# Kernel tuning notes

Hardware: AMD Instinct MI355X
Metric: run time of the kernel (lower is better)

Reference implementation:

```python
import jax, jax.numpy as jnp
import numpy as np

NEG = -1e9  # stand-in for -inf in masked softmax (safe under autodiff)

def setup_inputs() -> dict:
    key = jax.random.key(0)
    ks = jax.random.split(key, 10)
    B, Btot, O, M, F, Dsrc, Ddst = 32, 64, 1000, 100, 32, 6, 3
    raw_opes = jax.random.normal(ks[0], (B, O, Dsrc), jnp.float32)
    raw_mas = jax.random.normal(ks[1], (B, M, Ddst), jnp.float32)
    proc_time = jax.random.uniform(ks[2], (B, O, M), jnp.float32)
    ope_ma_adj = jax.random.randint(ks[3], (Btot, O, M), 0, 2).astype(jnp.int64)
    batch_idxes = jnp.sort(jax.random.randint(ks[4], (B,), 0, Btot)).astype(jnp.int64)
    # xavier-ish scaled params
    W_src = jax.random.normal(ks[5], (Dsrc, F), jnp.float32) * (2.0 / np.sqrt(Dsrc + F))
    W_dst = jax.random.normal(ks[6], (Ddst, F), jnp.float32) * (2.0 / np.sqrt(Ddst + F))
    W_edge = jax.random.normal(ks[7], (F,), jnp.float32) * (2.0 / np.sqrt(1 + F))
    attn_l = jax.random.normal(ks[8], (F,), jnp.float32) * (2.0 / np.sqrt(1 + F))
    attn_r = jax.random.normal(ks[9], (F,), jnp.float32) * (2.0 / np.sqrt(1 + F))
    return {"raw_opes": raw_opes, "raw_mas": raw_mas, "proc_time": proc_time,
            "ope_ma_adj": ope_ma_adj, "batch_idxes": batch_idxes,
            "W_src": W_src, "W_dst": W_dst, "W_edge": W_edge,
            "attn_l": attn_l, "attn_r": attn_r}

def _leaky(x, s=0.2):
    return jnp.where(x >= 0, x, s * x)

def reference(raw_opes, raw_mas, proc_time, ope_ma_adj, batch_idxes, W_src, W_dst, W_edge, attn_l, attn_r):
    adj = ope_ma_adj[batch_idxes]                      # [B,O,M] int
    adjf = adj.astype(raw_opes.dtype)
    feat_src = raw_opes @ W_src                        # [B,O,F]
    feat_dst = raw_mas @ W_dst                         # [B,M,F]
    feat_edge = proc_time[..., None] * W_edge          # [B,O,M,F]
    el = feat_src @ attn_l                             # [B,O]
    er = feat_dst @ attn_r                             # [B,M]
    ee = feat_edge @ attn_l                            # [B,O,M]  (original uses attn_l for edges)
    a = adjf * el[:, :, None] + ee + adjf * er[:, None, :]   # [B,O,M]
    eijk = _leaky(a)                                   # [B,O,M]
    ekk = _leaky(er + er)                              # [B,M]
    e = jnp.concatenate([eijk, ekk[:, None, :]], axis=1)     # [B,O+1,M]
    mask = jnp.concatenate([adj == 1, jnp.ones_like(adj[:, :1, :], dtype=bool)], axis=1)
    e = jnp.where(mask, e, NEG)
    alpha = jax.nn.softmax(e, axis=1)                  # softmax over ope dim (+self)
    alpha_ijk = alpha[:, :-1, :]                       # [B,O,M]
    alpha_kk = alpha[:, -1, :]                         # [B,M]
    Wmu_ijk = feat_edge + feat_src[:, :, None, :]      # [B,O,M,F]
    b = jnp.einsum('bomf,bom->bmf', Wmu_ijk, alpha_ijk)
    c = feat_dst * alpha_kk[..., None]
    return jax.nn.sigmoid(b + c)                       # [B,M,F]
```

## Files before the change

kernel.cpp:

```cpp
#include <hip/hip_runtime.h>

#define B_DIM 32
#define O_DIM 1000
#define M_DIM 100
#define F_DIM 32
#define DS 6
#define DD 3
#define SEG 25
#define CHUNK 40
#define OSUB 10
#define TRIPS 4
#define MT 25

__global__ __launch_bounds__(256) void gat_partial(
    const float* __restrict__ raw_opes,
    const float* __restrict__ raw_mas,
    const float* __restrict__ proc_time,
    const int*   __restrict__ adj,
    const int*   __restrict__ bidx,
    const float* __restrict__ Wsrc,
    const float* __restrict__ Wdst,
    const float* __restrict__ Wedge,
    const float* __restrict__ attn_l,
    const float* __restrict__ attn_r,
    float* __restrict__ partial)
{
    const int b   = blockIdx.x / SEG;
    const int seg = blockIdx.x % SEG;
    const int t   = threadIdx.x;
    const int o0  = seg * CHUNK;

    __shared__ float ro_s[CHUNK * DS];
    __shared__ float part_s[OSUB][M_DIM][9];
    __shared__ float wfold[10];

    const int mg = t % 25;
    const int g  = t / 25;

    float4 pt[TRIPS];
    int4   av[TRIPS];
    if (t < 25 * OSUB) {
        const float* ptp = proc_time + ((size_t)b * O_DIM + o0) * M_DIM + mg * 4;
        #pragma unroll
        for (int k = 0; k < TRIPS; ++k)
            pt[k] = *(const float4*)(ptp + (g + k * OSUB) * M_DIM);
        const int* adp = adj + ((size_t)bidx[b] * O_DIM + o0) * M_DIM + mg * 4;
        #pragma unroll
        for (int k = 0; k < TRIPS; ++k)
            av[k] = *(const int4*)(adp + (g + k * OSUB) * M_DIM);
    }

    const float* rop = raw_opes + ((size_t)b * O_DIM + o0) * DS;
    if (t < CHUNK * DS) ro_s[t] = rop[t];

    if (t >= 192) {
        const int l = t - 192;
        const int f = l & 31;
        float al = attn_l[f], ar = attn_r[f];
        float p[10];
        #pragma unroll
        for (int d = 0; d < DS; ++d) p[d] = Wsrc[d * F_DIM + f] * al;
        p[6] = Wedge[f] * al;
        #pragma unroll
        for (int d = 0; d < DD; ++d) p[7 + d] = Wdst[d * F_DIM + f] * ar;
        #pragma unroll
        for (int s = 1; s < 32; s <<= 1) {
            #pragma unroll
            for (int k = 0; k < 10; ++k) p[k] += __shfl_xor(p[k], s);
        }
        if (l == 0) {
            #pragma unroll
            for (int k = 0; k < 10; ++k) wfold[k] = p[k];
        }
    }
    __syncthreads();

    if (t < 25 * OSUB) {
        float wl[DS], wr[DD], we;
        #pragma unroll
        for (int d = 0; d < DS; ++d) wl[d] = wfold[d];
        we = wfold[6];
        #pragma unroll
        for (int d = 0; d < DD; ++d) wr[d] = wfold[7 + d];

        const float* rm = raw_mas + ((size_t)b * M_DIM + mg * 4) * DD;
        float4 er;
        er.x = fmaf(rm[0], wr[0], fmaf(rm[1],  wr[1], rm[2]  * wr[2]));
        er.y = fmaf(rm[3], wr[0], fmaf(rm[4],  wr[1], rm[5]  * wr[2]));
        er.z = fmaf(rm[6], wr[0], fmaf(rm[7],  wr[1], rm[8]  * wr[2]));
        er.w = fmaf(rm[9], wr[0], fmaf(rm[10], wr[1], rm[11] * wr[2]));

        float4 den = make_float4(0, 0, 0, 0), spa = make_float4(0, 0, 0, 0);
        float4 sd[DS];
        #pragma unroll
        for (int d = 0; d < DS; ++d) sd[d] = make_float4(0, 0, 0, 0);

        #pragma unroll
        for (int k = 0; k < TRIPS; ++k) {
            const int row = g + k * OSUB;
            float ro[DS];
            #pragma unroll
            for (int d = 0; d < DS; ++d) ro[d] = ro_s[row * DS + d];
            float elr = 0.f;
            #pragma unroll
            for (int d = 0; d < DS; ++d) elr = fmaf(ro[d], wl[d], elr);

            float s0 = elr + er.x + we * pt[k].x;
            float s1 = elr + er.y + we * pt[k].y;
            float s2 = elr + er.z + we * pt[k].z;
            float s3 = elr + er.w + we * pt[k].w;
            s0 = fmaxf(s0, 0.2f * s0); s1 = fmaxf(s1, 0.2f * s1);
            s2 = fmaxf(s2, 0.2f * s2); s3 = fmaxf(s3, 0.2f * s3);
            float p0 = (av[k].x == 1) ? __expf(s0) : 0.f;
            float p1 = (av[k].y == 1) ? __expf(s1) : 0.f;
            float p2 = (av[k].z == 1) ? __expf(s2) : 0.f;
            float p3 = (av[k].w == 1) ? __expf(s3) : 0.f;
            den.x += p0; den.y += p1; den.z += p2; den.w += p3;
            spa.x = fmaf(p0, pt[k].x, spa.x); spa.y = fmaf(p1, pt[k].y, spa.y);
            spa.z = fmaf(p2, pt[k].z, spa.z); spa.w = fmaf(p3, pt[k].w, spa.w);
            #pragma unroll
            for (int d = 0; d < DS; ++d) {
                sd[d].x = fmaf(p0, ro[d], sd[d].x);
                sd[d].y = fmaf(p1, ro[d], sd[d].y);
                sd[d].z = fmaf(p2, ro[d], sd[d].z);
                sd[d].w = fmaf(p3, ro[d], sd[d].w);
            }
        }

        #pragma unroll
        for (int j = 0; j < 4; ++j) {
            const int m = mg * 4 + j;
            float* ps = part_s[g][m];
            ps[0] = j == 0 ? den.x : j == 1 ? den.y : j == 2 ? den.z : den.w;
            ps[1] = j == 0 ? spa.x : j == 1 ? spa.y : j == 2 ? spa.z : spa.w;
            #pragma unroll
            for (int d = 0; d < DS; ++d)
                ps[2 + d] = j == 0 ? sd[d].x : j == 1 ? sd[d].y : j == 2 ? sd[d].z : sd[d].w;
        }
    }
    __syncthreads();

    if (t < 2 * M_DIM) {
        const int m = t % M_DIM, half = t / M_DIM;
        float a[4] = {0, 0, 0, 0};
        #pragma unroll
        for (int gg = 0; gg < OSUB; ++gg) {
            #pragma unroll
            for (int k = 0; k < 4; ++k) a[k] += part_s[gg][m][half * 4 + k];
        }
        *(float4*)(partial + (((size_t)b * SEG + seg) * M_DIM + m) * 8 + half * 4) =
            make_float4(a[0], a[1], a[2], a[3]);
    }
}

__global__ __launch_bounds__(256) void gat_final(
    const float* __restrict__ raw_mas,
    const float* __restrict__ Wsrc,
    const float* __restrict__ Wdst,
    const float* __restrict__ Wedge,
    const float* __restrict__ attn_r,
    const float* __restrict__ partial,
    float* __restrict__ out)
{
    const int b  = blockIdx.x >> 2;
    const int m0 = (blockIdx.x & 3) * MT;
    const int t  = threadIdx.x;

    __shared__ float smd[MT][9];
    __shared__ float wr_s[DD];

    if (t >= 192) {
        const int l = t - 192;
        const int f = l & 31;
        float ar = attn_r[f];
        float p[DD];
        #pragma unroll
        for (int d = 0; d < DD; ++d) p[d] = Wdst[d * F_DIM + f] * ar;
        #pragma unroll
        for (int s = 1; s < 32; s <<= 1) {
            #pragma unroll
            for (int d = 0; d < DD; ++d) p[d] += __shfl_xor(p[d], s);
        }
        if (l == 0) {
            #pragma unroll
            for (int d = 0; d < DD; ++d) wr_s[d] = p[d];
        }
    }

    if (t < MT * 8) {
        const int ml = t % MT;
        const int k  = t / MT;
        const float* p = partial + (((size_t)b * SEG) * M_DIM + m0 + ml) * 8 + k;
        float acc = 0.f;
        #pragma unroll
        for (int s = 0; s < SEG; ++s) acc += p[(size_t)s * M_DIM * 8];
        smd[ml][k] = acc;
    }
    __syncthreads();

    if (t < MT) {
        const float* rm = raw_mas + ((size_t)b * M_DIM + m0 + t) * DD;
        float er = fmaf(rm[0], wr_s[0], fmaf(rm[1], wr_s[1], rm[2] * wr_s[2]));
        float skk = 2.f * er;
        skk = fmaxf(skk, 0.2f * skk);
        float pkk = __expf(skk);
        float den = smd[t][0], spa = smd[t][1];
        float s0 = smd[t][2], s1 = smd[t][3], s2 = smd[t][4],
              s3 = smd[t][5], s4 = smd[t][6], s5 = smd[t][7];
        float inv = 1.f / (den + pkk);
        smd[t][0] = s0 * inv; smd[t][1] = s1 * inv; smd[t][2] = s2 * inv;
        smd[t][3] = s3 * inv; smd[t][4] = s4 * inv; smd[t][5] = s5 * inv;
        smd[t][6] = spa * inv;
        smd[t][7] = pkk * inv;
    }
    __syncthreads();

    for (int idx = t; idx < MT * F_DIM; idx += 256) {
        const int ml = idx >> 5;
        const int f  = idx & 31;
        float v = smd[ml][6] * Wedge[f];
        #pragma unroll
        for (int d = 0; d < DS; ++d) v = fmaf(smd[ml][d], Wsrc[d * F_DIM + f], v);
        const float* rm = raw_mas + ((size_t)b * M_DIM + m0 + ml) * DD;
        float fd = 0.f;
        #pragma unroll
        for (int d = 0; d < DD; ++d) fd = fmaf(rm[d], Wdst[d * F_DIM + f], fd);
        v = fmaf(fd, smd[ml][7], v);
        out[((size_t)b * M_DIM + m0 + ml) * F_DIM + f] = 1.f / (1.f + __expf(-v));
    }
}

extern "C" void kernel_launch(void* const* d_in, const int* in_sizes, int n_in,
                              void* d_out, int out_size, void* d_ws, size_t ws_size,
                              hipStream_t stream) {
    const float* raw_opes  = (const float*)d_in[0];
    const float* raw_mas   = (const float*)d_in[1];
    const float* proc_time = (const float*)d_in[2];
    const int*   adj       = (const int*)d_in[3];
    const int*   bidx      = (const int*)d_in[4];
    const float* Wsrc      = (const float*)d_in[5];
    const float* Wdst      = (const float*)d_in[6];
    const float* Wedge     = (const float*)d_in[7];
    const float* attn_l    = (const float*)d_in[8];
    const float* attn_r    = (const float*)d_in[9];
    float* out     = (float*)d_out;
    float* partial = (float*)d_ws;

    gat_partial<<<B_DIM * SEG, 256, 0, stream>>>(raw_opes, raw_mas, proc_time, adj, bidx,
                                                 Wsrc, Wdst, Wedge, attn_l, attn_r, partial);
    gat_final<<<B_DIM * 4, 256, 0, stream>>>(raw_mas, Wsrc, Wdst, Wedge, attn_r, partial, out);
}
```

Measured before the change: 17.11 us.

## Reduce segment partials with atomics and flatten final kernel per output element

Each segment block now atomically adds its per-machine partial sums into a zeroed accumulator, replacing the per-segment partial buffer. The memset that zeroes it adds an extra operation to the stream. Segment 0 also writes er to a buffer, so the final kernel becomes a flat one-thread-per-output elementwise pass without shared memory, the cross-segment loop, or the attn_r reduction. The intent is to remove the final kernel's serial 25-way reduction and its synchronisations. In exchange it adds atomic contention on 8 values per (b,m) and makes the floating-point summation order nondeterministic.

Result: slower. 36.25 us (+111.9%).

```diff
diff --git a/kernel.cpp b/kernel.cpp
--- a/kernel.cpp
+++ b/kernel.cpp
@@ -10,7 +10,8 @@
 #define CHUNK 40
 #define OSUB 10
 #define TRIPS 4
-#define MT 25
+#define ACC_BYTES ((size_t)B_DIM * M_DIM * 8 * sizeof(float))
+#define ER_BYTES  ((size_t)B_DIM * M_DIM * sizeof(float))
 
 __global__ __launch_bounds__(256) void gat_partial(
     const float* __restrict__ raw_opes,
@@ -23,7 +24,8 @@
     const float* __restrict__ Wedge,
     const float* __restrict__ attn_l,
     const float* __restrict__ attn_r,
-    float* __restrict__ partial)
+    float* __restrict__ accum,
+    float* __restrict__ er_buf)
 {
     const int b   = blockIdx.x / SEG;
     const int seg = blockIdx.x % SEG;
@@ -89,6 +91,11 @@
         er.y = fmaf(rm[3], wr[0], fmaf(rm[4],  wr[1], rm[5]  * wr[2]));
         er.z = fmaf(rm[6], wr[0], fmaf(rm[7],  wr[1], rm[8]  * wr[2]));
         er.w = fmaf(rm[9], wr[0], fmaf(rm[10], wr[1], rm[11] * wr[2]));
+
+        if (seg == 0 && g == 0) {
+            float* eb = er_buf + (size_t)b * M_DIM + mg * 4;
+            eb[0] = er.x; eb[1] = er.y; eb[2] = er.z; eb[3] = er.w;
+        }
 
         float4 den = make_float4(0, 0, 0, 0), spa = make_float4(0, 0, 0, 0);
         float4 sd[DS];
@@ -148,8 +155,9 @@
             #pragma unroll
             for (int k = 0; k < 4; ++k) a[k] += part_s[gg][m][half * 4 + k];
         }
-        *(float4*)(partial + (((size_t)b * SEG + seg) * M_DIM + m) * 8 + half * 4) =
-            make_float4(a[0], a[1], a[2], a[3]);
+        float* dst = accum + ((size_t)b * M_DIM + m) * 8 + half * 4;
+        #pragma unroll
+        for (int k = 0; k < 4; ++k) atomicAdd(dst + k, a[k]);
     }
 }
 
@@ -158,76 +166,38 @@
     const float* __restrict__ Wsrc,
     const float* __restrict__ Wdst,
     const float* __restrict__ Wedge,
-    const float* __restrict__ attn_r,
-    const float* __restrict__ partial,
+    const float* __restrict__ accum,
+    const float* __restrict__ er_buf,
     float* __restrict__ out)
 {
-    const int b  = blockIdx.x >> 2;
-    const int m0 = (blockIdx.x & 3) * MT;
-    const int t  = threadIdx.x;
-
-    __shared__ float smd[MT][9];
-    __shared__ float wr_s[DD];
-
-    if (t >= 192) {
-        const int l = t - 192;
-        const int f = l & 31;
-        float ar = attn_r[f];
-        float p[DD];
-        #pragma unroll
-        for (int d = 0; d < DD; ++d) p[d] = Wdst[d * F_DIM + f] * ar;
-        #pragma unroll
-        for (int s = 1; s < 32; s <<= 1) {
-            #pragma unroll
-            for (int d = 0; d < DD; ++d) p[d] += __shfl_xor(p[d], s);
-        }
-        if (l == 0) {
-            #pragma unroll
-            for (int d = 0; d < DD; ++d) wr_s[d] = p[d];
-        }
-    }
-
-    if (t < MT * 8) {
-        const int ml = t % MT;
-        const int k  = t / MT;
-        const float* p = partial + (((size_t)b * SEG) * M_DIM + m0 + ml) * 8 + k;
-        float acc = 0.f;
-        #pragma unroll
-        for (int s = 0; s < SEG; ++s) acc += p[(size_t)s * M_DIM * 8];
-        smd[ml][k] = acc;
-    }
-    __syncthreads();
-
-    if (t < MT) {
-        const float* rm = raw_mas + ((size_t)b * M_DIM + m0 + t) * DD;
-        float er = fmaf(rm[0], wr_s[0], fmaf(rm[1], wr_s[1], rm[2] * wr_s[2]));
-        float skk = 2.f * er;
-        skk = fmaxf(skk, 0.2f * skk);
-        float pkk = __expf(skk);
-        float den = smd[t][0], spa = smd[t][1];
-        float s0 = smd[t][2], s1 = smd[t][3], s2 = smd[t][4],
-              s3 = smd[t][5], s4 = smd[t][6], s5 = smd[t][7];
-        float inv = 1.f / (den + pkk);
-        smd[t][0] = s0 * inv; smd[t][1] = s1 * inv; smd[t][2] = s2 * inv;
-        smd[t][3] = s3 * inv; smd[t][4] = s4 * inv; smd[t][5] = s5 * inv;
-        smd[t][6] = spa * inv;
-        smd[t][7] = pkk * inv;
-    }
-    __syncthreads();
-
-    for (int idx = t; idx < MT * F_DIM; idx += 256) {
-        const int ml = idx >> 5;
-        const int f  = idx & 31;
-        float v = smd[ml][6] * Wedge[f];
-        #pragma unroll
-        for (int d = 0; d < DS; ++d) v = fmaf(smd[ml][d], Wsrc[d * F_DIM + f], v);
-        const float* rm = raw_mas + ((size_t)b * M_DIM + m0 + ml) * DD;
-        float fd = 0.f;
-        #pragma unroll
-        for (int d = 0; d < DD; ++d) fd = fmaf(rm[d], Wdst[d * F_DIM + f], fd);
-        v = fmaf(fd, smd[ml][7], v);
-        out[((size_t)b * M_DIM + m0 + ml) * F_DIM + f] = 1.f / (1.f + __expf(-v));
-    }
+    const int idx = blockIdx.x * 256 + threadIdx.x;
+    const int f   = idx & 31;
+    const int bm  = idx >> 5;
+
+    const float4 a0 = *(const float4*)(accum + (size_t)bm * 8);
+    const float4 a1 = *(const float4*)(accum + (size_t)bm * 8 + 4);
+    const float  er = er_buf[bm];
+
+    float skk = 2.f * er;
+    skk = fmaxf(skk, 0.2f * skk);
+    float pkk = __expf(skk);
+    float inv = 1.f / (a0.x + pkk);
+
+    float v = a0.y * inv * Wedge[f];
+    v = fmaf(a0.z * inv, Wsrc[0 * F_DIM + f], v);
+    v = fmaf(a0.w * inv, Wsrc[1 * F_DIM + f], v);
+    v = fmaf(a1.x * inv, Wsrc[2 * F_DIM + f], v);
+    v = fmaf(a1.y * inv, Wsrc[3 * F_DIM + f], v);
+    v = fmaf(a1.z * inv, Wsrc[4 * F_DIM + f], v);
+    v = fmaf(a1.w * inv, Wsrc[5 * F_DIM + f], v);
+
+    const float* rm = raw_mas + (size_t)bm * DD;
+    float fd = rm[0] * Wdst[0 * F_DIM + f];
+    fd = fmaf(rm[1], Wdst[1 * F_DIM + f], fd);
+    fd = fmaf(rm[2], Wdst[2 * F_DIM + f], fd);
+    v = fmaf(fd, pkk * inv, v);
+
+    out[(size_t)bm * F_DIM + f] = 1.f / (1.f + __expf(-v));
 }
 
 extern "C" void kernel_launch(void* const* d_in, const int* in_sizes, int n_in,
@@ -243,10 +213,14 @@
     const float* Wedge     = (const float*)d_in[7];
     const float* attn_l    = (const float*)d_in[8];
     const float* attn_r    = (const float*)d_in[9];
-    float* out     = (float*)d_out;
-    float* partial = (float*)d_ws;
-
+    float* out    = (float*)d_out;
+    float* accum  = (float*)d_ws;
+    float* er_buf = (float*)((char*)d_ws + ACC_BYTES);
+
+    hipMemsetAsync(accum, 0, ACC_BYTES + ER_BYTES, stream);
     gat_partial<<<B_DIM * SEG, 256, 0, stream>>>(raw_opes, raw_mas, proc_time, adj, bidx,
-                                                 Wsrc, Wdst, Wedge, attn_l, attn_r, partial);
-    gat_final<<<B_DIM * 4, 256, 0, stream>>>(raw_mas, Wsrc, Wdst, Wedge, attn_r, partial, out);
+                                                 Wsrc, Wdst, Wedge, attn_l, attn_r,
+                                                 accum, er_buf);
+    gat_final<<<(B_DIM * M_DIM * F_DIM) / 256, 256, 0, stream>>>(
+        raw_mas, Wsrc, Wdst, Wedge, accum, er_buf, out);
 }
```
